# Performance work log

Hardware: AMD Instinct MI355X
Metric: run time of the kernel (lower is better)

The kernel has to match this reference:

```python
import jax, jax.numpy as jnp
import numpy as np

THETA = 10000.0
MASK_FILL = -60000.0

def _rope(x):
    # lucidrains rotary_embedding_torch semantics: interleaved pairs, full-dim rotation
    S, D = x.shape[-2], x.shape[-1]
    inv_freq = 1.0 / (THETA ** (jnp.arange(0, D, 2, dtype=jnp.float32) / D))  # [D/2]
    freqs = jnp.arange(S, dtype=jnp.float32)[:, None] * inv_freq[None, :]     # [S, D/2]
    freqs = jnp.repeat(freqs, 2, axis=-1)                                     # [S, D] (each freq twice)
    cos, sin = jnp.cos(freqs), jnp.sin(freqs)
    xr = x.reshape(x.shape[:-1] + (D // 2, 2))
    rot_half = jnp.stack((-xr[..., 1], xr[..., 0]), axis=-1).reshape(x.shape)  # (x1,x2)->(-x2,x1)
    return x * cos + rot_half * sin

def setup_inputs() -> dict:
    key = jax.random.key(0)
    kq, kk, kv, km = jax.random.split(key, 4)
    B, H, S, D = 4, 16, 2048, 128
    return {
        "query": jax.random.normal(kq, (B, H, S, D), dtype=jnp.float32),
        "key": jax.random.normal(kk, (B, H, S, D), dtype=jnp.float32),
        "value": jax.random.normal(kv, (B, H, S, D), dtype=jnp.float32),
        "mask": jax.random.randint(km, (1, 1, S, S), 0, 2, dtype=jnp.int32),
    }

def reference(query, key, value, mask):
    q = _rope(query)
    k = _rope(key)
    scale = 1.0 / jnp.sqrt(jnp.float32(q.shape[-1]))
    scores = jnp.einsum('bhqd,bhkd->bhqk', q, k) * scale
    scores = jnp.where(mask == 0, jnp.float32(MASK_FILL), scores)
    p_attn = jax.nn.softmax(scores, axis=-1)
    out = jnp.einsum('bhqk,bhkd->bhqd', p_attn, value)
    return out, p_attn
```

## Files before the change

kernel.cpp:

```cpp
#include <hip/hip_runtime.h>
#include <hip/hip_fp16.h>
#include <cstdint>
#include <cstddef>

#define Bn 4
#define Hn 16
#define Sn 2048
#define Dn 128
#define MSHIFT 8.0f

typedef _Float16 half8  __attribute__((ext_vector_type(8)));
typedef float    f32x16 __attribute__((ext_vector_type(16)));
typedef float    f32x4v __attribute__((ext_vector_type(4)));
typedef unsigned uint4v __attribute__((ext_vector_type(4)));

__device__ __forceinline__ int pk_f16(float a, float b){
  auto h = __builtin_amdgcn_cvt_pkrtz(a, b);
  return __builtin_bit_cast(int, h);
}


__global__ void k_prep0(float2* __restrict__ tab,
                        const int* __restrict__ mask, unsigned* __restrict__ mtb){
  const int bid = blockIdx.x;
  if (bid < 512){
    const int idx = bid*256 + threadIdx.x;
    const int i = idx & 63, s = idx >> 6;
    const double invf = exp(-(double)i * (9.210340371976184 / 64.0));
    const double ang  = (double)s * invf;
    float2 cs; cs.x = (float)cos(ang); cs.y = (float)sin(ang);
    tab[idx] = cs;
  } else {
    const int g = (bid - 512)*256 + threadIdx.x;
    const int k = g & (Sn-1), q32 = g >> 11;
    unsigned bits = 0u;
    for (int j = 0; j < 32; ++j)
      bits |= (mask[(size_t)(q32*32 + j)*Sn + k] != 0 ? 1u : 0u) << j;
    mtb[g] = bits;
  }
}


__global__ void k_pack(const float* __restrict__ q, const float* __restrict__ k,
                       const float* __restrict__ v, const float2* __restrict__ tab,
                       half8* __restrict__ qp, half8* __restrict__ kp,
                       half8* __restrict__ vp){
  const int bid = blockIdx.x;
  if (bid < 8192){
    const int t    = bid*256 + threadIdx.x;
    const int lane = t & 63, ln = lane & 31, h = lane >> 5;
    const int dc   = (t >> 6) & 7;
    const int blk  = (t >> 9) & 63;
    const int bh   = t >> 15;
    const int s    = blk*32 + ln;
    const size_t roff = ((size_t)bh*Sn + s)*Dn + dc*16 + h*8;
    const float4 a0 = *(const float4*)(q + roff);
    const float4 a1 = *(const float4*)(q + roff + 4);
    const float4 b0 = *(const float4*)(k + roff);
    const float4 b1 = *(const float4*)(k + roff + 4);
    const float2* tb = tab + s*64 + dc*8 + h*4;
    const float2 c0 = tb[0], c1 = tb[1], c2 = tb[2], c3 = tb[3];
    const float SC = 0.08838834764831845f;
    half8 qo, ko;
    qo[0] = (_Float16)((a0.x*c0.x - a0.y*c0.y)*SC);
    qo[1] = (_Float16)((a0.y*c0.x + a0.x*c0.y)*SC);
    qo[2] = (_Float16)((a0.z*c1.x - a0.w*c1.y)*SC);
    qo[3] = (_Float16)((a0.w*c1.x + a0.z*c1.y)*SC);
    qo[4] = (_Float16)((a1.x*c2.x - a1.y*c2.y)*SC);
    qo[5] = (_Float16)((a1.y*c2.x + a1.x*c2.y)*SC);
    qo[6] = (_Float16)((a1.z*c3.x - a1.w*c3.y)*SC);
    qo[7] = (_Float16)((a1.w*c3.x + a1.z*c3.y)*SC);
    ko[0] = (_Float16)(b0.x*c0.x - b0.y*c0.y);
    ko[1] = (_Float16)(b0.y*c0.x + b0.x*c0.y);
    ko[2] = (_Float16)(b0.z*c1.x - b0.w*c1.y);
    ko[3] = (_Float16)(b0.w*c1.x + b0.z*c1.y);
    ko[4] = (_Float16)(b1.x*c2.x - b1.y*c2.y);
    ko[5] = (_Float16)(b1.y*c2.x + b1.x*c2.y);
    ko[6] = (_Float16)(b1.z*c3.x - b1.w*c3.y);
    ko[7] = (_Float16)(b1.w*c3.x + b1.z*c3.y);
    qp[t] = qo;
    kp[t] = ko;
  } else {
    const int t    = (bid - 8192)*256 + threadIdx.x;
    const int lane = t & 63, ln = lane & 31, h = lane >> 5;
    const int dt   = (t >> 6) & 3;
    const int k16  = (t >> 8) & 127;
    const int bh   = t >> 15;
    const size_t base = ((size_t)bh*Sn + k16*16 + h*8)*Dn + dt*32 + ln;
    half8 o;
#pragma unroll
    for (int j = 0; j < 8; ++j) o[j] = (_Float16)v[base + (size_t)j*Dn];
    vp[t] = o;
  }
}


__global__ __launch_bounds__(512, 2) void attn_ps2(
    const half8* __restrict__ qp, const half8* __restrict__ kp,
    const unsigned* __restrict__ mtb, half8* __restrict__ wfrag,
    float* __restrict__ rinvb)
{
  const int bid  = blockIdx.x;
  const int work = ((bid & 7) << 6) + (bid >> 3);
  const int bh   = work >> 3;
  const int qg   = work & 7;
  const int w    = threadIdx.x >> 6;
  const int l    = threadIdx.x & 63;
  const int ln   = l & 31;
  const int h    = l >> 5;
  const int qb   = qg*8 + w;
  const int strip = bh*64 + qb;

  half8 qf[8];
#pragma unroll
  for (int dc = 0; dc < 8; ++dc)
    qf[dc] = qp[(((size_t)bh*64 + qb)*8 + dc)*64 + l];

  const unsigned* mrow = mtb + (size_t)qb*Sn;
  half8* wbase = wfrag + (size_t)strip*128*64;
  float L = 0.f;

  for (int kt = 0; kt < 64; ++kt){
    const half8* kf = kp + (((size_t)bh*64 + kt)*8)*64 + l;
    f32x16 a;
#pragma unroll
    for (int i = 0; i < 16; ++i) a[i] = 0.f;
#pragma unroll
    for (int dc = 0; dc < 8; ++dc)
      a = __builtin_amdgcn_mfma_f32_32x32x16_f16(kf[(size_t)dc*64], qf[dc], a, 0, 0, 0);

#pragma unroll
    for (int mm = 0; mm < 4; ++mm){
      const uint4v dw = *(const uint4v*)(mrow + kt*32 + mm*8 + h*4);
#pragma unroll
      for (int aa = 0; aa < 4; ++aa){
        const int r = mm*4 + aa;
        const float s = ((dw[aa] >> ln) & 1u) ? a[r] : -1.0e30f;
        const float u = __expf(s - MSHIFT);
        a[r] = u;
        L += u;
      }
    }

    int pk2[4][2];
#pragma unroll
    for (int b = 0; b < 4; ++b){
      pk2[b][0] = pk_f16(a[4*b+0], a[4*b+1]);
      pk2[b][1] = pk_f16(a[4*b+2], a[4*b+3]);
    }

#pragma unroll
    for (int t16 = 0; t16 < 2; ++t16){
      const int P00 = pk2[2*t16+0][0];
      const int P01 = pk2[2*t16+0][1];
      const int P10 = pk2[2*t16+1][0];
      const int P11 = pk2[2*t16+1][1];
      const int S00 = __shfl_xor(P00, 32, 64);
      const int S01 = __shfl_xor(P01, 32, 64);
      const int S10 = __shfl_xor(P10, 32, 64);
      const int S11 = __shfl_xor(P11, 32, 64);
      int4 bi;
      bi.x = h ? S10 : P00;
      bi.y = h ? S11 : P01;
      bi.z = h ? P10 : S00;
      bi.w = h ? P11 : S01;
      wbase[(size_t)(kt*2 + t16)*64 + l] = __builtin_bit_cast(half8, bi);
    }
  }

  L += __shfl_xor(L, 32, 64);
  if (l < 32) rinvb[(size_t)strip*32 + ln] = 1.0f / L;
}


__global__ __launch_bounds__(512, 2) void attn_o(
    const half8* __restrict__ vp, const half8* __restrict__ wfrag,
    const float* __restrict__ rinvb, float* __restrict__ out)
{
  __shared__ float pt[8][32][34];

  const int bid  = blockIdx.x;
  const int work = 511 - (((bid & 7) << 6) + (bid >> 3));
  const int bh   = work >> 3;
  const int qg   = work & 7;
  const int w    = threadIdx.x >> 6;
  const int l    = threadIdx.x & 63;
  const int ln   = l & 31;
  const int h    = l >> 5;
  const int qb   = qg*8 + w;
  const int strip = bh*64 + qb;

  f32x16 oacc[4];
#pragma unroll
  for (int dt = 0; dt < 4; ++dt)
#pragma unroll
    for (int i = 0; i < 16; ++i) oacc[dt][i] = 0.f;

  const half8* wbase = wfrag + (size_t)strip*128*64;
  const half8* vbase = vp + (size_t)bh*128*4*64;

#pragma unroll 4
  for (int ks = 0; ks < 128; ++ks){
    const half8 bf = wbase[(size_t)ks*64 + l];
    const half8* vf = vbase + (size_t)ks*4*64 + l;
#pragma unroll
    for (int dt = 0; dt < 4; ++dt)
      oacc[dt] = __builtin_amdgcn_mfma_f32_32x32x16_f16(vf[(size_t)dt*64], bf, oacc[dt], 0, 0, 0);
  }

  const float rinv = rinvb[(size_t)strip*32 + ln];
#pragma unroll
  for (int dt = 0; dt < 4; ++dt)
#pragma unroll
    for (int i = 0; i < 16; ++i) oacc[dt][i] *= rinv;

  const size_t obase = ((size_t)bh*Sn + qb*32)*Dn;
  const int rq = l >> 3;
  const int rc = (l & 7) * 4;
#pragma unroll
  for (int dt = 0; dt < 4; ++dt){
#pragma unroll
    for (int g = 0; g < 4; ++g){
      const int c = g*8 + h*4;
      float2 e0, e1;
      e0.x = oacc[dt][4*g+0]; e0.y = oacc[dt][4*g+1];
      e1.x = oacc[dt][4*g+2]; e1.y = oacc[dt][4*g+3];
      *(float2*)&pt[w][ln][c]   = e0;
      *(float2*)&pt[w][ln][c+2] = e1;
    }
#pragma unroll
    for (int i = 0; i < 4; ++i){
      const int qq = i*8 + rq;
      const float2 t0 = *(const float2*)&pt[w][qq][rc];
      const float2 t1 = *(const float2*)&pt[w][qq][rc+2];
      f32x4v o4; o4.x = t0.x; o4.y = t0.y; o4.z = t1.x; o4.w = t1.y;
      __builtin_nontemporal_store(o4, (f32x4v*)(out + obase + (size_t)qq*Dn + dt*32 + rc));
    }
  }
}


__global__ __launch_bounds__(512, 2) void k_expand(
    const half8* __restrict__ wfrag, const float* __restrict__ rinvb,
    float* __restrict__ pout)
{
  __shared__ _Float16 ps[32][1032];
  __shared__ float rv[32];

  const int b     = blockIdx.x;
  const int strip = b >> 1;
  const int hh    = b & 1;
  const int tid   = threadIdx.x;
  const int l     = tid & 63;
  const int w8    = tid >> 6;
  const int ln    = l & 31;
  const int h     = l >> 5;

  if (tid < 32) rv[tid] = rinvb[(size_t)strip*32 + tid];

#pragma unroll
  for (int i = 0; i < 8; ++i){
    const int cc = w8*8 + i;
    const half8 v = wfrag[((size_t)strip*128 + hh*64 + cc)*64 + l];
    *(half8*)&ps[ln][cc*16 + h*8] = v;
  }
  __syncthreads();

  const int bh = strip >> 6, qb = strip & 63;
  float* dst0 = pout + ((size_t)bh*Sn + qb*32)*Sn + hh*1024;
#pragma unroll
  for (int it = 0; it < 8; ++it){
    const int id  = it*512 + tid;
    const int row = id >> 7;
    const int c   = (id & 127) * 8;
    const half8 hv = *(const half8*)&ps[row][c];
    const float r = rv[row];
    f32x4v v0, v1;
    v0.x = (float)hv[0]*r; v0.y = (float)hv[1]*r; v0.z = (float)hv[2]*r; v0.w = (float)hv[3]*r;
    v1.x = (float)hv[4]*r; v1.y = (float)hv[5]*r; v1.z = (float)hv[6]*r; v1.w = (float)hv[7]*r;
    float* dp = dst0 + (size_t)row*Sn + c;
    __builtin_nontemporal_store(v0, (f32x4v*)dp);
    __builtin_nontemporal_store(v1, (f32x4v*)(dp + 4));
  }
}


extern "C" void kernel_launch(void* const* d_in, const int* in_sizes, int n_in,
                              void* d_out, int out_size, void* d_ws, size_t ws_size,
                              hipStream_t stream)
{
  const float* dq = (const float*)d_in[0];
  const float* dk = (const float*)d_in[1];
  const float* dv = (const float*)d_in[2];
  const int*   dm = (const int*)d_in[3];

  char* ws = (char*)d_ws;
  float2*   tab  = (float2*)ws;
  half8*    qp   = (half8*)(ws + (size_t)(1u<<20));
  half8*    kp   = (half8*)(ws + (size_t)(1u<<20) + ((size_t)32<<20));
  half8*    vp   = (half8*)(ws + (size_t)(1u<<20) + ((size_t)64<<20));
  unsigned* mtb  = (unsigned*)(ws + (size_t)(1u<<20) + ((size_t)96<<20));
  float*    rinvb= (float*)(ws + (size_t)(1u<<20) + ((size_t)97<<20));
  half8*    wfr  = (half8*)(ws + (size_t)(1u<<20) + ((size_t)98<<20));

  float* out  = (float*)d_out;
  float* pout = out + (size_t)Bn*Hn*Sn*Dn;

  k_prep0  <<<1024,  256, 0, stream>>>(tab, dm, mtb);
  k_pack   <<<16384, 256, 0, stream>>>(dq, dk, dv, tab, qp, kp, vp);
  attn_ps2 <<<512,   512, 0, stream>>>(qp, kp, mtb, wfr, rinvb);
  attn_o   <<<512,   512, 0, stream>>>(vp, wfr, rinvb, out);
  k_expand <<<8192,  512, 0, stream>>>(wfr, rinvb, pout);
}
```

Measured before the change: 1.021 ms.

## Merge PV output and probability expansion kernels into one interleaved launch

Fuses the attn_o MFMA kernel and the k_expand probability writer into a single launch of 8704 blocks, where every 17th block does the P·V output work and the rest expand probabilities to fp32. The intent is to overlap the compute-bound PV blocks with the store-bandwidth-bound expansion blocks and to remove one launch and its tail. The cost is that the PV branch now shares the larger LDS allocation, which may reduce occupancy, and block-role divergence adds some imbalance.

```diff
diff --git a/kernel.cpp b/kernel.cpp
--- a/kernel.cpp
+++ b/kernel.cpp
@@ -173,114 +173,111 @@
 }
 
 
-__global__ __launch_bounds__(512, 2) void attn_o(
+__global__ __launch_bounds__(512, 2) void attn_ox(
     const half8* __restrict__ vp, const half8* __restrict__ wfrag,
-    const float* __restrict__ rinvb, float* __restrict__ out)
-{
-  __shared__ float pt[8][32][34];
-
-  const int bid  = blockIdx.x;
-  const int work = 511 - (((bid & 7) << 6) + (bid >> 3));
-  const int bh   = work >> 3;
-  const int qg   = work & 7;
-  const int w    = threadIdx.x >> 6;
-  const int l    = threadIdx.x & 63;
-  const int ln   = l & 31;
-  const int h    = l >> 5;
-  const int qb   = qg*8 + w;
-  const int strip = bh*64 + qb;
-
-  f32x16 oacc[4];
-#pragma unroll
-  for (int dt = 0; dt < 4; ++dt)
-#pragma unroll
-    for (int i = 0; i < 16; ++i) oacc[dt][i] = 0.f;
-
-  const half8* wbase = wfrag + (size_t)strip*128*64;
-  const half8* vbase = vp + (size_t)bh*128*4*64;
-
-#pragma unroll 4
-  for (int ks = 0; ks < 128; ++ks){
-    const half8 bf = wbase[(size_t)ks*64 + l];
-    const half8* vf = vbase + (size_t)ks*4*64 + l;
-#pragma unroll
-    for (int dt = 0; dt < 4; ++dt)
-      oacc[dt] = __builtin_amdgcn_mfma_f32_32x32x16_f16(vf[(size_t)dt*64], bf, oacc[dt], 0, 0, 0);
-  }
-
-  const float rinv = rinvb[(size_t)strip*32 + ln];
-#pragma unroll
-  for (int dt = 0; dt < 4; ++dt)
-#pragma unroll
-    for (int i = 0; i < 16; ++i) oacc[dt][i] *= rinv;
-
-  const size_t obase = ((size_t)bh*Sn + qb*32)*Dn;
-  const int rq = l >> 3;
-  const int rc = (l & 7) * 4;
-#pragma unroll
-  for (int dt = 0; dt < 4; ++dt){
-#pragma unroll
-    for (int g = 0; g < 4; ++g){
-      const int c = g*8 + h*4;
-      float2 e0, e1;
-      e0.x = oacc[dt][4*g+0]; e0.y = oacc[dt][4*g+1];
-      e1.x = oacc[dt][4*g+2]; e1.y = oacc[dt][4*g+3];
-      *(float2*)&pt[w][ln][c]   = e0;
-      *(float2*)&pt[w][ln][c+2] = e1;
-    }
-#pragma unroll
-    for (int i = 0; i < 4; ++i){
-      const int qq = i*8 + rq;
-      const float2 t0 = *(const float2*)&pt[w][qq][rc];
-      const float2 t1 = *(const float2*)&pt[w][qq][rc+2];
-      f32x4v o4; o4.x = t0.x; o4.y = t0.y; o4.z = t1.x; o4.w = t1.y;
-      __builtin_nontemporal_store(o4, (f32x4v*)(out + obase + (size_t)qq*Dn + dt*32 + rc));
-    }
-  }
-}
-
-
-__global__ __launch_bounds__(512, 2) void k_expand(
-    const half8* __restrict__ wfrag, const float* __restrict__ rinvb,
+    const float* __restrict__ rinvb, float* __restrict__ out,
     float* __restrict__ pout)
 {
   __shared__ _Float16 ps[32][1032];
   __shared__ float rv[32];
 
-  const int b     = blockIdx.x;
-  const int strip = b >> 1;
-  const int hh    = b & 1;
-  const int tid   = threadIdx.x;
-  const int l     = tid & 63;
-  const int w8    = tid >> 6;
-  const int ln    = l & 31;
-  const int h     = l >> 5;
-
-  if (tid < 32) rv[tid] = rinvb[(size_t)strip*32 + tid];
-
-#pragma unroll
-  for (int i = 0; i < 8; ++i){
-    const int cc = w8*8 + i;
-    const half8 v = wfrag[((size_t)strip*128 + hh*64 + cc)*64 + l];
-    *(half8*)&ps[ln][cc*16 + h*8] = v;
-  }
-  __syncthreads();
-
-  const int bh = strip >> 6, qb = strip & 63;
-  float* dst0 = pout + ((size_t)bh*Sn + qb*32)*Sn + hh*1024;
-#pragma unroll
-  for (int it = 0; it < 8; ++it){
-    const int id  = it*512 + tid;
-    const int row = id >> 7;
-    const int c   = (id & 127) * 8;
-    const half8 hv = *(const half8*)&ps[row][c];
-    const float r = rv[row];
-    f32x4v v0, v1;
-    v0.x = (float)hv[0]*r; v0.y = (float)hv[1]*r; v0.z = (float)hv[2]*r; v0.w = (float)hv[3]*r;
-    v1.x = (float)hv[4]*r; v1.y = (float)hv[5]*r; v1.z = (float)hv[6]*r; v1.w = (float)hv[7]*r;
-    float* dp = dst0 + (size_t)row*Sn + c;
-    __builtin_nontemporal_store(v0, (f32x4v*)dp);
-    __builtin_nontemporal_store(v1, (f32x4v*)(dp + 4));
+  const int bid = blockIdx.x;
+  const int tid = threadIdx.x;
+  const int l   = tid & 63;
+  const int ln  = l & 31;
+  const int h   = l >> 5;
+
+  if (bid % 17 == 0){
+    const int o_id = bid / 17;
+    const int work = 511 - (((o_id & 7) << 6) + (o_id >> 3));
+    const int bh   = work >> 3;
+    const int qg   = work & 7;
+    const int w    = tid >> 6;
+    const int qb   = qg*8 + w;
+    const int strip = bh*64 + qb;
+    float* pt = (float*)&ps[0][0];
+    #define PT(W,Q,C) pt[(((W)*32 + (Q))*34) + (C)]
+
+    f32x16 oacc[4];
+#pragma unroll
+    for (int dt = 0; dt < 4; ++dt)
+#pragma unroll
+      for (int i = 0; i < 16; ++i) oacc[dt][i] = 0.f;
+
+    const half8* wbase = wfrag + (size_t)strip*128*64;
+    const half8* vbase = vp + (size_t)bh*128*4*64;
+
+#pragma unroll 4
+    for (int ks = 0; ks < 128; ++ks){
+      const half8 bf = wbase[(size_t)ks*64 + l];
+      const half8* vf = vbase + (size_t)ks*4*64 + l;
+#pragma unroll
+      for (int dt = 0; dt < 4; ++dt)
+        oacc[dt] = __builtin_amdgcn_mfma_f32_32x32x16_f16(vf[(size_t)dt*64], bf, oacc[dt], 0, 0, 0);
+    }
+
+    const float rinv = rinvb[(size_t)strip*32 + ln];
+#pragma unroll
+    for (int dt = 0; dt < 4; ++dt)
+#pragma unroll
+      for (int i = 0; i < 16; ++i) oacc[dt][i] *= rinv;
+
+    const size_t obase = ((size_t)bh*Sn + qb*32)*Dn;
+    const int rq = l >> 3;
+    const int rc = (l & 7) * 4;
+#pragma unroll
+    for (int dt = 0; dt < 4; ++dt){
+#pragma unroll
+      for (int g = 0; g < 4; ++g){
+        const int c = g*8 + h*4;
+        float2 e0, e1;
+        e0.x = oacc[dt][4*g+0]; e0.y = oacc[dt][4*g+1];
+        e1.x = oacc[dt][4*g+2]; e1.y = oacc[dt][4*g+3];
+        *(float2*)&PT(w, ln, c)   = e0;
+        *(float2*)&PT(w, ln, c+2) = e1;
+      }
+#pragma unroll
+      for (int i = 0; i < 4; ++i){
+        const int qq = i*8 + rq;
+        const float2 t0 = *(const float2*)&PT(w, qq, rc);
+        const float2 t1 = *(const float2*)&PT(w, qq, rc+2);
+        f32x4v o4; o4.x = t0.x; o4.y = t0.y; o4.z = t1.x; o4.w = t1.y;
+        __builtin_nontemporal_store(o4, (f32x4v*)(out + obase + (size_t)qq*Dn + dt*32 + rc));
+      }
+    }
+    #undef PT
+  } else {
+    const int e_id  = bid - bid/17 - 1;
+    const int strip = e_id >> 1;
+    const int hh    = e_id & 1;
+    const int w8    = tid >> 6;
+
+    if (tid < 32) rv[tid] = rinvb[(size_t)strip*32 + tid];
+
+#pragma unroll
+    for (int i = 0; i < 8; ++i){
+      const int cc = w8*8 + i;
+      const half8 v = wfrag[((size_t)strip*128 + hh*64 + cc)*64 + l];
+      *(half8*)&ps[ln][cc*16 + h*8] = v;
+    }
+    __syncthreads();
+
+    const int bh = strip >> 6, qb = strip & 63;
+    float* dst0 = pout + ((size_t)bh*Sn + qb*32)*Sn + hh*1024;
+#pragma unroll
+    for (int it = 0; it < 8; ++it){
+      const int id  = it*512 + tid;
+      const int row = id >> 7;
+      const int c   = (id & 127) * 8;
+      const half8 hv = *(const half8*)&ps[row][c];
+      const float r = rv[row];
+      f32x4v v0, v1;
+      v0.x = (float)hv[0]*r; v0.y = (float)hv[1]*r; v0.z = (float)hv[2]*r; v0.w = (float)hv[3]*r;
+      v1.x = (float)hv[4]*r; v1.y = (float)hv[5]*r; v1.z = (float)hv[6]*r; v1.w = (float)hv[7]*r;
+      float* dp = dst0 + (size_t)row*Sn + c;
+      __builtin_nontemporal_store(v0, (f32x4v*)dp);
+      __builtin_nontemporal_store(v1, (f32x4v*)(dp + 4));
+    }
   }
 }
 
@@ -309,6 +306,5 @@
   k_prep0  <<<1024,  256, 0, stream>>>(tab, dm, mtb);
   k_pack   <<<16384, 256, 0, stream>>>(dq, dk, dv, tab, qp, kp, vp);
   attn_ps2 <<<512,   512, 0, stream>>>(qp, kp, mtb, wfr, rinvb);
-  attn_o   <<<512,   512, 0, stream>>>(vp, wfr, rinvb, out);
-  k_expand <<<8192,  512, 0, stream>>>(wfr, rinvb, pout);
-}
+  attn_ox  <<<8704,  512, 0, stream>>>(vp, wfr, rinvb, out, pout);
+}
```

After: 893.9 us. 12.5% less time.
